# Kernel optimization log

Measured on AMD Instinct MI355X. Metric: run time of the kernel, lower is better.

The kernel has to match this reference:

```python
import jax, jax.numpy as jnp
import numpy as np

N = 16384
H = 256
C = 2


def setup_inputs() -> dict:
    key = jax.random.key(0)
    ks = jax.random.split(key, 9)
    s = lambda fan_in: 1.0 / np.sqrt(fan_in)
    return {
        "coordinates": jax.random.normal(ks[0], (N, C), dtype=jnp.float32) * 10.0,
        "W1": jax.random.normal(ks[1], (C, H), dtype=jnp.float32) * s(C),
        "b1": jnp.zeros((H,), dtype=jnp.float32),
        "W2": jax.random.normal(ks[2], (H, H), dtype=jnp.float32) * s(H),
        "b2": jnp.zeros((H,), dtype=jnp.float32),
        "Wd1": jax.random.normal(ks[3], (1, H // 2), dtype=jnp.float32) * s(1),
        "bd1": jnp.zeros((H // 2,), dtype=jnp.float32),
        "Wd2": jax.random.normal(ks[4], (H // 2, H), dtype=jnp.float32) * s(H // 2),
        "bd2": jnp.zeros((H,), dtype=jnp.float32),
        "k": 6,
    }


def reference(coordinates, W1, b1, W2, b2, Wd1, bd1, Wd2, bd2, k):
    x = coordinates.astype(jnp.float32)
    # coord MLP: Linear -> SiLU -> Linear
    coord_emb = jax.nn.silu(x @ W1 + b1) @ W2 + b2  # (N, H)

    # pairwise Euclidean distances (N, N), via ||a||^2 + ||b||^2 - 2ab
    sq = jnp.sum(x * x, axis=1)  # (N,)
    d2 = sq[:, None] + sq[None, :] - 2.0 * (x @ x.T)
    dist = jnp.sqrt(jnp.maximum(d2, 1e-12))  # safe sqrt; diag ~ 0

    # k+1 smallest distances per row (includes self at ~0), ascending
    kk = min(k + 1, dist.shape[1])
    neg_top, _ = jax.lax.top_k(-dist, kk)
    topk_dist = -neg_top  # ascending smallest
    mean_dist = jnp.mean(topk_dist[:, 1:], axis=1, keepdims=True)  # (N, 1)

    dist_emb = jax.nn.silu(mean_dist @ Wd1 + bd1) @ Wd2 + bd2  # (N, H)
    return coord_emb + dist_emb
```

## Files before the change

### kernel.cpp

```cpp
#include <hip/hip_runtime.h>
#include <float.h>
#include <math.h>

#define NPTS 16384
#define HDIM 256

#define KNB   256
#define KXMIN (-48.0f)
#define KW    0.375f
#define KINVW (1.0f / KW)
#define NHB   32

typedef __attribute__((ext_vector_type(8))) short bf16x8;
typedef __attribute__((ext_vector_type(4))) float f32x4;

__device__ __forceinline__ float silu_f(float z) {
    return z / (1.0f + __expf(-z));
}

__device__ __forceinline__ short f2bf(float f) {
    unsigned u = __float_as_uint(f);
    u = (u + 0x7FFFu + ((u >> 16) & 1u)) >> 16;
    return (short)u;
}

__device__ __forceinline__ float bcast_lane(float x, int l) {
    return __int_as_float(__builtin_amdgcn_readlane(__float_as_int(x), l));
}

__device__ __forceinline__ int binof(float x) {
    int b = (int)floorf((x - KXMIN) * KINVW);
    return b < 0 ? 0 : (b > KNB - 1 ? KNB - 1 : b);
}

#define INS7(a0,a1,a2,a3,a4,a5,a6,V)                \
    {   const float v_ = (V);                       \
        a6 = fmaxf(a5, fminf(a6, v_));              \
        a5 = fmaxf(a4, fminf(a5, v_));              \
        a4 = fmaxf(a3, fminf(a4, v_));              \
        a3 = fmaxf(a2, fminf(a3, v_));              \
        a2 = fmaxf(a1, fminf(a2, v_));              \
        a1 = fmaxf(a0, fminf(a1, v_));              \
        a0 = fminf(a0, v_);                         \
    }

__global__ __launch_bounds__(256) void hist_kernel(const float* __restrict__ xyf,
                                                   unsigned* __restrict__ histp) {
    __shared__ unsigned lh[KNB];
    lh[threadIdx.x] = 0u;
    __syncthreads();
    for (int i = blockIdx.x * 256 + threadIdx.x; i < NPTS; i += NHB * 256)
        atomicAdd(&lh[binof(xyf[2 * i])], 1u);
    __syncthreads();
    histp[blockIdx.x * KNB + threadIdx.x] = lh[threadIdx.x];
}

__global__ __launch_bounds__(256) void scan_kernel(const unsigned* __restrict__ histp,
                                                   unsigned* __restrict__ off,
                                                   unsigned* __restrict__ cursor) {
    __shared__ unsigned sh[KNB];
    const int tid = threadIdx.x;
    unsigned own = 0;
    #pragma unroll
    for (int b = 0; b < NHB; ++b) own += histp[b * KNB + tid];
    sh[tid] = own;
    __syncthreads();
    for (int s = 1; s < KNB; s <<= 1) {
        const unsigned v = (tid >= s) ? sh[tid - s] : 0u;
        __syncthreads();
        sh[tid] += v;
        __syncthreads();
    }
    const unsigned excl = sh[tid] - own;
    off[tid]    = excl;
    cursor[tid] = excl;
    if (tid == KNB - 1) off[KNB] = (unsigned)NPTS;
}

__global__ __launch_bounds__(256) void scatter_kernel(const float* __restrict__ xyf,
                                                      unsigned* __restrict__ cursor,
                                                      float2* __restrict__ sxy,
                                                      unsigned* __restrict__ qidx) {
    for (int i = blockIdx.x * 256 + threadIdx.x; i < NPTS; i += NHB * 256) {
        const float2 p = ((const float2*)xyf)[i];
        const unsigned pos = atomicAdd(&cursor[binof(p.x)], 1u);
        sxy[pos]  = p;
        qidx[pos] = (unsigned)i;
    }
}

__global__ __launch_bounds__(512, 8) void knn_search(const float2* __restrict__ sxy,
                                                     const unsigned* __restrict__ qidx,
                                                     const unsigned* __restrict__ off,
                                                     float* __restrict__ md) {
    const int lane = threadIdx.x & 63;
    const int wv   = threadIdx.x >> 6;
    const int qpos = blockIdx.x * 8 + wv;
    const float2 q = sxy[qpos];

    float s0 = FLT_MAX, s1 = FLT_MAX, s2 = FLT_MAX, s3 = FLT_MAX,
          s4 = FLT_MAX, s5 = FLT_MAX, s6 = FLT_MAX;

    const int b0 = binof(q.x);
    const int lb = b0 > 0 ? b0 - 1 : 0;
    const int rb = b0 < KNB - 1 ? b0 + 1 : KNB - 1;

    {
        const unsigned o = off[lb], e = off[rb + 1];
        for (unsigned u = o + (unsigned)lane; u < e; u += 64u) {
            const float2 p = sxy[u];
            const float dx = q.x - p.x, dy = q.y - p.y;
            const float d2 = fmaf(dx, dx, dy * dy);
            if (d2 < s6) INS7(s0, s1, s2, s3, s4, s5, s6, d2)
        }
    }

    float g0 = FLT_MAX, g1 = FLT_MAX, g2 = FLT_MAX, g3 = FLT_MAX,
          g4 = FLT_MAX, g5 = FLT_MAX, g6 = FLT_MAX;
    {
        unsigned long long m = __ballot(s0 < g6);
        while (m) {
            const int L   = __ffsll(m) - 1;
            const float v = bcast_lane(s0, L);
            INS7(g0, g1, g2, g3, g4, g5, g6, v)
            if (lane == L) {
                s0 = s1; s1 = s2; s2 = s3; s3 = s4; s4 = s5; s5 = s6;
                s6 = FLT_MAX;
            }
            m = __ballot(s0 < g6);
        }
    }

    int l = lb - 1, r = rb + 1;
    while (l >= 0 || r < KNB) {
        float bl = FLT_MAX, br = FLT_MAX;
        if (l >= 0) {
            const float d = fmaxf(q.x - (KXMIN + (float)(l + 1) * KW), 0.0f);
            bl = d * d;
        }
        if (r < KNB) {
            const float d = fmaxf((KXMIN + (float)r * KW) - q.x, 0.0f);
            br = d * d;
        }
        if (fminf(bl, br) > g6) break;
        const int b = (bl <= br) ? l : r;
        const unsigned o = off[b], e = off[b + 1];
        for (unsigned u = o; u < e; u += 64u) {
            const unsigned idx = u + (unsigned)lane;
            float d2 = FLT_MAX;
            if (idx < e) {
                const float2 p = sxy[idx];
                const float dx = q.x - p.x, dy = q.y - p.y;
                d2 = fmaf(dx, dx, dy * dy);
            }
            unsigned long long m = __ballot(d2 < g6);
            while (m) {
                const int L   = __ffsll(m) - 1;
                const float v = bcast_lane(d2, L);
                INS7(g0, g1, g2, g3, g4, g5, g6, v)
                if (lane == L) d2 = FLT_MAX;
                m = __ballot(d2 < g6);
            }
        }
        if (bl <= br) --l; else ++r;
    }

    if (lane == 0) {
        const float sum = sqrtf(fmaxf(g1, 1e-12f)) + sqrtf(fmaxf(g2, 1e-12f)) +
                          sqrtf(fmaxf(g3, 1e-12f)) + sqrtf(fmaxf(g4, 1e-12f)) +
                          sqrtf(fmaxf(g5, 1e-12f)) + sqrtf(fmaxf(g6, 1e-12f));
        md[qidx[qpos]] = sum * (1.0f / 6.0f);
    }
}

__global__ __launch_bounds__(256) void pack_kernel(const float* __restrict__ W2,
                                                   const float* __restrict__ Wd2,
                                                   unsigned short* __restrict__ W2p,
                                                   unsigned short* __restrict__ Wd2p) {
    const int slot = blockIdx.x * 256 + threadIdx.x;
    const float* src;
    unsigned short* dst;
    int s;
    if (slot < 8192) { src = W2;  dst = W2p;  s = slot; }
    else             { src = Wd2; dst = Wd2p; s = slot - 8192; }
    const int t   = s >> 10;
    const int rem = s & 1023;
    const int ct  = rem >> 6;
    const int l   = rem & 63;
    const int k0  = t * 32 + 8 * (l >> 4);
    const int c   = ct * 16 + (l & 15);
    bf16x8 v;
    #pragma unroll
    for (int i = 0; i < 8; ++i)
        v[i] = f2bf(src[(size_t)(k0 + i) * HDIM + c]);
    ((bf16x8*)dst)[s] = v;
}

#define GEN_A(T)                                                              \
    {                                                                         \
        const int kb = (T) * 32 + klane;                                      \
        const float4 p0 = *(const float4*)(W1 + kb);                          \
        const float4 p1 = *(const float4*)(W1 + kb + 4);                      \
        const float4 r0_ = *(const float4*)(W1 + HDIM + kb);                  \
        const float4 r1_ = *(const float4*)(W1 + HDIM + kb + 4);              \
        const float4 c0_ = *(const float4*)(b1 + kb);                         \
        const float4 c1_ = *(const float4*)(b1 + kb + 4);                     \
        const float pw[8] = {p0.x,p0.y,p0.z,p0.w,p1.x,p1.y,p1.z,p1.w};        \
        const float rw[8] = {r0_.x,r0_.y,r0_.z,r0_.w,r1_.x,r1_.y,r1_.z,r1_.w};\
        const float cw[8] = {c0_.x,c0_.y,c0_.z,c0_.w,c1_.x,c1_.y,c1_.z,c1_.w};\
        _Pragma("unroll")                                                     \
        for (int i = 0; i < 8; ++i)                                           \
            a[i] = f2bf(silu_f(fmaf(q.x, pw[i], fmaf(q.y, rw[i], cw[i]))));   \
    }

#define GEN_G(T)                                                              \
    {                                                                         \
        const int kb = (T) * 32 + klane;                                      \
        const float4 p0 = *(const float4*)(Wd1 + kb);                         \
        const float4 p1 = *(const float4*)(Wd1 + kb + 4);                     \
        const float4 c0_ = *(const float4*)(bd1 + kb);                        \
        const float4 c1_ = *(const float4*)(bd1 + kb + 4);                    \
        const float pw[8] = {p0.x,p0.y,p0.z,p0.w,p1.x,p1.y,p1.z,p1.w};        \
        const float cw[8] = {c0_.x,c0_.y,c0_.z,c0_.w,c1_.x,c1_.y,c1_.z,c1_.w};\
        _Pragma("unroll")                                                     \
        for (int i = 0; i < 8; ++i)                                           \
            a[i] = f2bf(silu_f(fmaf(mdr, pw[i], cw[i])));                     \
    }

#define MFMA8(BUF)                                                            \
    _Pragma("unroll")                                                         \
    for (int j = 0; j < 8; ++j)                                               \
        acc[j] = __builtin_amdgcn_mfma_f32_16x16x32_bf16(a, BUF[j], acc[j], 0, 0, 0);

#define LOADB(BUF, ARR, T)                                                    \
    _Pragma("unroll")                                                         \
    for (int j = 0; j < 8; ++j)                                               \
        BUF[j] = ARR[((T) * 16 + ch * 8 + j) * 64 + lane];

__global__ __launch_bounds__(256, 2) void mlp_kernel(
        const float* __restrict__ xyf,
        const float* __restrict__ W1,  const float* __restrict__ b1,
        const float* __restrict__ b2,
        const float* __restrict__ Wd1, const float* __restrict__ bd1,
        const float* __restrict__ bd2,
        const unsigned short* __restrict__ W2p,
        const unsigned short* __restrict__ Wd2p,
        const float* __restrict__ md,  float* __restrict__ out) {
    const int tid  = threadIdx.x;
    const int lane = tid & 63;
    const int w    = tid >> 6;
    const int r0   = blockIdx.x * 32 + (w >> 1) * 16;
    const int ch   = w & 1;
    const int row  = r0 + (lane & 15);
    const float2 q = ((const float2*)xyf)[row];
    const float mdr = md[row];
    const int klane = 8 * (lane >> 4);

    f32x4 acc[8];
    #pragma unroll
    for (int j = 0; j < 8; ++j) {
        acc[j][0] = 0.0f; acc[j][1] = 0.0f; acc[j][2] = 0.0f; acc[j][3] = 0.0f;
    }

    const bf16x8* B1 = (const bf16x8*)W2p;
    const bf16x8* B2 = (const bf16x8*)Wd2p;
    bf16x8 bA[8], bB[8];
    bf16x8 a;

    LOADB(bA, B1, 0)

    #pragma unroll
    for (int tt = 0; tt < 4; ++tt) {
        {   const int t = 2 * tt;
            GEN_A(t)
            LOADB(bB, B1, t + 1)
            MFMA8(bA)
        }
        {   const int t = 2 * tt + 1;
            GEN_A(t)
            if (t + 1 < 8) { LOADB(bA, B1, t + 1) }
            else           { LOADB(bA, B2, 0)     }
            MFMA8(bB)
        }
    }

    #pragma unroll
    for (int uu = 0; uu < 2; ++uu) {
        {   const int t = 2 * uu;
            GEN_G(t)
            LOADB(bB, B2, t + 1)
            MFMA8(bA)
        }
        {   const int t = 2 * uu + 1;
            GEN_G(t)
            if (t + 1 < 4) { LOADB(bA, B2, t + 1) }
            MFMA8(bB)
        }
    }

    const int cb = ch * 128;
    const int rr = r0 + 4 * (lane >> 4);
    #pragma unroll
    for (int j = 0; j < 8; ++j) {
        const int c = cb + j * 16 + (lane & 15);
        const float add = b2[c] + bd2[c];
        out[(size_t)(rr + 0) * HDIM + c] = acc[j][0] + add;
        out[(size_t)(rr + 1) * HDIM + c] = acc[j][1] + add;
        out[(size_t)(rr + 2) * HDIM + c] = acc[j][2] + add;
        out[(size_t)(rr + 3) * HDIM + c] = acc[j][3] + add;
    }
}

extern "C" void kernel_launch(void* const* d_in, const int* in_sizes, int n_in,
                              void* d_out, int out_size, void* d_ws, size_t ws_size,
                              hipStream_t stream) {
    const float* xy  = (const float*)d_in[0];
    const float* W1  = (const float*)d_in[1];
    const float* b1  = (const float*)d_in[2];
    const float* W2  = (const float*)d_in[3];
    const float* b2  = (const float*)d_in[4];
    const float* Wd1 = (const float*)d_in[5];
    const float* bd1 = (const float*)d_in[6];
    const float* Wd2 = (const float*)d_in[7];
    const float* bd2 = (const float*)d_in[8];
    float* out = (float*)d_out;

    char* ws = (char*)d_ws;
    float*          md     = (float*)ws;
    unsigned short* W2p    = (unsigned short*)(ws + 65536);
    unsigned short* Wd2p   = (unsigned short*)(ws + 196608);
    unsigned*       histp  = (unsigned*)(ws + 262144);
    unsigned*       off    = (unsigned*)(ws + 294912);
    unsigned*       cursor = (unsigned*)(ws + 296192);
    float2*         sxy    = (float2*)(ws + 297216);
    unsigned*       qidx   = (unsigned*)(ws + 428288);

    hist_kernel<<<NHB, 256, 0, stream>>>(xy, histp);
    scan_kernel<<<1, 256, 0, stream>>>(histp, off, cursor);
    scatter_kernel<<<NHB, 256, 0, stream>>>(xy, cursor, sxy, qidx);
    knn_search<<<NPTS / 8, 512, 0, stream>>>(sxy, qidx, off, md);
    pack_kernel<<<48, 256, 0, stream>>>(W2, Wd2, W2p, Wd2p);
    mlp_kernel<<<NPTS / 32, 256, 0, stream>>>(xy, W1, b1, b2, Wd1, bd1, bd2,
                                              W2p, Wd2p, md, out);
}
```

Measured before the change: 176.0 us.

## Fuse binning and weight packing into one prep kernel; butterfly-merge per-lane top-7

Merges the histogram, scan, scatter and weight-pack kernels into a single 13-block launch. Twelve blocks pack the weights and one 1024-thread block does the counting sort entirely in shared memory. This removes three kernel launches and the global partial-histogram round trip, but the scatter now runs on a single block. The serial ballot-based merge of per-lane top-7 lists is replaced with a 6-step xor-shuffle butterfly that merges sorted lists branch-free. All lanes then hold the same top-7, which the ring search reuses directly.

```diff
diff --git a/kernel.cpp b/kernel.cpp
--- a/kernel.cpp
+++ b/kernel.cpp
@@ -9,7 +9,6 @@
 #define KXMIN (-48.0f)
 #define KW    0.375f
 #define KINVW (1.0f / KW)
-#define NHB   32
 
 typedef __attribute__((ext_vector_type(8))) short bf16x8;
 typedef __attribute__((ext_vector_type(4))) float f32x4;
@@ -44,46 +43,63 @@
         a0 = fminf(a0, v_);                         \
     }
 
-__global__ __launch_bounds__(256) void hist_kernel(const float* __restrict__ xyf,
-                                                   unsigned* __restrict__ histp) {
-    __shared__ unsigned lh[KNB];
-    lh[threadIdx.x] = 0u;
+__global__ __launch_bounds__(1024) void prep_kernel(
+        const float* __restrict__ xyf,
+        const float* __restrict__ W2, const float* __restrict__ Wd2,
+        unsigned short* __restrict__ W2p, unsigned short* __restrict__ Wd2p,
+        float2* __restrict__ sxy, unsigned* __restrict__ qidx,
+        unsigned* __restrict__ off) {
+    const int tid = threadIdx.x;
+
+    if (blockIdx.x < 12) {
+        const int slot = blockIdx.x * 1024 + tid;
+        const float* src;
+        unsigned short* dst;
+        int s;
+        if (slot < 8192) { src = W2;  dst = W2p;  s = slot; }
+        else             { src = Wd2; dst = Wd2p; s = slot - 8192; }
+        const int t   = s >> 10;
+        const int rem = s & 1023;
+        const int ct  = rem >> 6;
+        const int l   = rem & 63;
+        const int k0  = t * 32 + 8 * (l >> 4);
+        const int c   = ct * 16 + (l & 15);
+        bf16x8 v;
+        #pragma unroll
+        for (int i = 0; i < 8; ++i)
+            v[i] = f2bf(src[(size_t)(k0 + i) * HDIM + c]);
+        ((bf16x8*)dst)[s] = v;
+        return;
+    }
+
+    __shared__ unsigned h[KNB];
+    __shared__ unsigned sc[KNB];
+    __shared__ unsigned cur[KNB];
+    if (tid < KNB) h[tid] = 0u;
     __syncthreads();
-    for (int i = blockIdx.x * 256 + threadIdx.x; i < NPTS; i += NHB * 256)
-        atomicAdd(&lh[binof(xyf[2 * i])], 1u);
+    for (int i = tid; i < NPTS; i += 1024)
+        atomicAdd(&h[binof(xyf[2 * i])], 1u);
     __syncthreads();
-    histp[blockIdx.x * KNB + threadIdx.x] = lh[threadIdx.x];
-}
-
-__global__ __launch_bounds__(256) void scan_kernel(const unsigned* __restrict__ histp,
-                                                   unsigned* __restrict__ off,
-                                                   unsigned* __restrict__ cursor) {
-    __shared__ unsigned sh[KNB];
-    const int tid = threadIdx.x;
-    unsigned own = 0;
-    #pragma unroll
-    for (int b = 0; b < NHB; ++b) own += histp[b * KNB + tid];
-    sh[tid] = own;
+    unsigned own = 0u;
+    if (tid < KNB) { own = h[tid]; sc[tid] = own; }
     __syncthreads();
     for (int s = 1; s < KNB; s <<= 1) {
-        const unsigned v = (tid >= s) ? sh[tid - s] : 0u;
+        unsigned v = 0u;
+        if (tid < KNB && tid >= s) v = sc[tid - s];
         __syncthreads();
-        sh[tid] += v;
+        if (tid < KNB) sc[tid] += v;
         __syncthreads();
     }
-    const unsigned excl = sh[tid] - own;
-    off[tid]    = excl;
-    cursor[tid] = excl;
-    if (tid == KNB - 1) off[KNB] = (unsigned)NPTS;
-}
-
-__global__ __launch_bounds__(256) void scatter_kernel(const float* __restrict__ xyf,
-                                                      unsigned* __restrict__ cursor,
-                                                      float2* __restrict__ sxy,
-                                                      unsigned* __restrict__ qidx) {
-    for (int i = blockIdx.x * 256 + threadIdx.x; i < NPTS; i += NHB * 256) {
+    if (tid < KNB) {
+        const unsigned excl = sc[tid] - own;
+        off[tid] = excl;
+        cur[tid] = excl;
+    }
+    if (tid == 0) off[KNB] = (unsigned)NPTS;
+    __syncthreads();
+    for (int i = tid; i < NPTS; i += 1024) {
         const float2 p = ((const float2*)xyf)[i];
-        const unsigned pos = atomicAdd(&cursor[binof(p.x)], 1u);
+        const unsigned pos = atomicAdd(&cur[binof(p.x)], 1u);
         sxy[pos]  = p;
         qidx[pos] = (unsigned)i;
     }
@@ -115,20 +131,36 @@
         }
     }
 
-    float g0 = FLT_MAX, g1 = FLT_MAX, g2 = FLT_MAX, g3 = FLT_MAX,
-          g4 = FLT_MAX, g5 = FLT_MAX, g6 = FLT_MAX;
-    {
-        unsigned long long m = __ballot(s0 < g6);
-        while (m) {
-            const int L   = __ffsll(m) - 1;
-            const float v = bcast_lane(s0, L);
-            INS7(g0, g1, g2, g3, g4, g5, g6, v)
-            if (lane == L) {
-                s0 = s1; s1 = s2; s2 = s3; s3 = s4; s4 = s5; s5 = s6;
-                s6 = FLT_MAX;
-            }
-            m = __ballot(s0 < g6);
-        }
+    #pragma unroll
+    for (int m = 1; m < 64; m <<= 1) {
+        const float o0 = __shfl_xor(s0, m);
+        const float o1 = __shfl_xor(s1, m);
+        const float o2 = __shfl_xor(s2, m);
+        const float o3 = __shfl_xor(s3, m);
+        const float o4 = __shfl_xor(s4, m);
+        const float o5 = __shfl_xor(s5, m);
+        const float o6 = __shfl_xor(s6, m);
+        const float n0 = fminf(s0, o0);
+        const float n1 = fminf(fminf(s1, o1), fmaxf(s0, o0));
+        const float n2 = fminf(fminf(s2, o2),
+                               fminf(fmaxf(s0, o1), fmaxf(s1, o0)));
+        const float n3 = fminf(fminf(s3, o3),
+                               fminf(fmaxf(s0, o2),
+                                     fminf(fmaxf(s1, o1), fmaxf(s2, o0))));
+        const float n4 = fminf(fminf(s4, o4),
+                               fminf(fminf(fmaxf(s0, o3), fmaxf(s1, o2)),
+                                     fminf(fmaxf(s2, o1), fmaxf(s3, o0))));
+        const float n5 = fminf(fminf(s5, o5),
+                               fminf(fminf(fmaxf(s0, o4), fmaxf(s1, o3)),
+                                     fminf(fmaxf(s2, o2),
+                                           fminf(fmaxf(s3, o1), fmaxf(s4, o0)))));
+        const float n6 = fminf(fminf(s6, o6),
+                               fminf(fminf(fmaxf(s0, o5), fmaxf(s1, o4)),
+                                     fminf(fmaxf(s2, o3),
+                                           fminf(fmaxf(s3, o2),
+                                                 fminf(fmaxf(s4, o1),
+                                                       fmaxf(s5, o0))))));
+        s0 = n0; s1 = n1; s2 = n2; s3 = n3; s4 = n4; s5 = n5; s6 = n6;
     }
 
     int l = lb - 1, r = rb + 1;
@@ -142,7 +174,7 @@
             const float d = fmaxf((KXMIN + (float)r * KW) - q.x, 0.0f);
             br = d * d;
         }
-        if (fminf(bl, br) > g6) break;
+        if (fminf(bl, br) > s6) break;
         const int b = (bl <= br) ? l : r;
         const unsigned o = off[b], e = off[b + 1];
         for (unsigned u = o; u < e; u += 64u) {
@@ -153,47 +185,24 @@
                 const float dx = q.x - p.x, dy = q.y - p.y;
                 d2 = fmaf(dx, dx, dy * dy);
             }
-            unsigned long long m = __ballot(d2 < g6);
+            unsigned long long m = __ballot(d2 < s6);
             while (m) {
                 const int L   = __ffsll(m) - 1;
                 const float v = bcast_lane(d2, L);
-                INS7(g0, g1, g2, g3, g4, g5, g6, v)
+                INS7(s0, s1, s2, s3, s4, s5, s6, v)
                 if (lane == L) d2 = FLT_MAX;
-                m = __ballot(d2 < g6);
+                m = __ballot(d2 < s6);
             }
         }
         if (bl <= br) --l; else ++r;
     }
 
     if (lane == 0) {
-        const float sum = sqrtf(fmaxf(g1, 1e-12f)) + sqrtf(fmaxf(g2, 1e-12f)) +
-                          sqrtf(fmaxf(g3, 1e-12f)) + sqrtf(fmaxf(g4, 1e-12f)) +
-                          sqrtf(fmaxf(g5, 1e-12f)) + sqrtf(fmaxf(g6, 1e-12f));
+        const float sum = sqrtf(fmaxf(s1, 1e-12f)) + sqrtf(fmaxf(s2, 1e-12f)) +
+                          sqrtf(fmaxf(s3, 1e-12f)) + sqrtf(fmaxf(s4, 1e-12f)) +
+                          sqrtf(fmaxf(s5, 1e-12f)) + sqrtf(fmaxf(s6, 1e-12f));
         md[qidx[qpos]] = sum * (1.0f / 6.0f);
     }
-}
-
-__global__ __launch_bounds__(256) void pack_kernel(const float* __restrict__ W2,
-                                                   const float* __restrict__ Wd2,
-                                                   unsigned short* __restrict__ W2p,
-                                                   unsigned short* __restrict__ Wd2p) {
-    const int slot = blockIdx.x * 256 + threadIdx.x;
-    const float* src;
-    unsigned short* dst;
-    int s;
-    if (slot < 8192) { src = W2;  dst = W2p;  s = slot; }
-    else             { src = Wd2; dst = Wd2p; s = slot - 8192; }
-    const int t   = s >> 10;
-    const int rem = s & 1023;
-    const int ct  = rem >> 6;
-    const int l   = rem & 63;
-    const int k0  = t * 32 + 8 * (l >> 4);
-    const int c   = ct * 16 + (l & 15);
-    bf16x8 v;
-    #pragma unroll
-    for (int i = 0; i < 8; ++i)
-        v[i] = f2bf(src[(size_t)(k0 + i) * HDIM + c]);
-    ((bf16x8*)dst)[s] = v;
 }
 
 #define GEN_A(T)                                                              \
@@ -326,20 +335,15 @@
     float* out = (float*)d_out;
 
     char* ws = (char*)d_ws;
-    float*          md     = (float*)ws;
-    unsigned short* W2p    = (unsigned short*)(ws + 65536);
-    unsigned short* Wd2p   = (unsigned short*)(ws + 196608);
-    unsigned*       histp  = (unsigned*)(ws + 262144);
-    unsigned*       off    = (unsigned*)(ws + 294912);
-    unsigned*       cursor = (unsigned*)(ws + 296192);
-    float2*         sxy    = (float2*)(ws + 297216);
-    unsigned*       qidx   = (unsigned*)(ws + 428288);
-
-    hist_kernel<<<NHB, 256, 0, stream>>>(xy, histp);
-    scan_kernel<<<1, 256, 0, stream>>>(histp, off, cursor);
-    scatter_kernel<<<NHB, 256, 0, stream>>>(xy, cursor, sxy, qidx);
+    float*          md   = (float*)ws;
+    unsigned short* W2p  = (unsigned short*)(ws + 65536);
+    unsigned short* Wd2p = (unsigned short*)(ws + 196608);
+    unsigned*       off  = (unsigned*)(ws + 262144);
+    float2*         sxy  = (float2*)(ws + 263424);
+    unsigned*       qidx = (unsigned*)(ws + 394496);
+
+    prep_kernel<<<13, 1024, 0, stream>>>(xy, W2, Wd2, W2p, Wd2p, sxy, qidx, off);
     knn_search<<<NPTS / 8, 512, 0, stream>>>(sxy, qidx, off, md);
-    pack_kernel<<<48, 256, 0, stream>>>(W2, Wd2, W2p, Wd2p);
     mlp_kernel<<<NPTS / 32, 256, 0, stream>>>(xy, W1, b1, b2, Wd1, bd1, bd2,
                                               W2p, Wd2p, md, out);
 }
```

After: 168.5 us. 1.04x faster.
